# Kernel optimization log

Hardware: AMD Instinct MI355X
Metric: run time of the kernel (lower is better)

## Reference

```python
import jax, jax.numpy as jnp
import numpy as np

N, E, D, O = 50000, 800000, 128, 128
BN_EPS = 1e-5

def setup_inputs() -> dict:
    key = jax.random.key(0)
    ks = jax.random.split(key, 12)
    s1 = 1.0 / np.sqrt(D)
    s2 = 1.0 / np.sqrt(O)
    return {
        "x": jax.random.normal(ks[0], (N, D), dtype=jnp.float32),
        "edge_index": jax.random.randint(ks[1], (2, E), 0, N, dtype=jnp.int64),
        "batch": jnp.zeros((N,), dtype=jnp.int64),
        "eps": jnp.float32(0.0),  # GINConv train_eps parameter, init 0
        "W1": jax.random.uniform(ks[2], (O, D), jnp.float32, -s1, s1),
        "b1": jax.random.uniform(ks[3], (O,), jnp.float32, -s1, s1),
        "gamma1": jnp.ones((O,), jnp.float32),
        "beta1": jnp.zeros((O,), jnp.float32),
        "W2": jax.random.uniform(ks[4], (O, O), jnp.float32, -s2, s2),
        "b2": jax.random.uniform(ks[5], (O,), jnp.float32, -s2, s2),
        "gamma2": jnp.ones((O,), jnp.float32),
        "beta2": jnp.zeros((O,), jnp.float32),
    }

def _bn(h, gamma, beta):
    # BatchNorm1d training mode: biased variance over nodes
    m = jnp.mean(h, axis=0)
    v = jnp.var(h, axis=0)
    return (h - m) * jax.lax.rsqrt(v + BN_EPS) * gamma + beta

def reference(x, edge_index, batch, eps, W1, b1, gamma1, beta1, W2, b2, gamma2, beta2):
    src, dst = edge_index[0], edge_index[1]
    # sum_{j in N(i)} x_j  (scatter-add over edges)
    agg = jax.ops.segment_sum(x[src], dst, num_segments=N)
    h = (1.0 + eps) * x + agg
    h = jax.nn.relu(_bn(h @ W1.T + b1, gamma1, beta1))
    h = jax.nn.relu(_bn(h @ W2.T + b2, gamma2, beta2))
    return h
```

## Files before the change

kernel.cpp:

```cpp
#include <hip/hip_runtime.h>
#include <hip/hip_bf16.h>

typedef __hip_bfloat16 bf16;
typedef unsigned short u16;
typedef unsigned int u32;
typedef __attribute__((ext_vector_type(8))) short short8;
typedef __attribute__((ext_vector_type(4))) float floatx4;

#define N_NODES 50000
#define N_EDGES 800000
#define DIM 128
#define NB2 1563
#define NB2A 1792
#define CAP2 768
#define T_EDGES 4096

__device__ __forceinline__ u16 f2bfbits(float f) {
    bf16 h = __float2bfloat16(f);
    return *(u16*)&h;
}
__device__ __forceinline__ unsigned pack2(float a, float b) {
    return (unsigned)f2bfbits(a) | ((unsigned)f2bfbits(b) << 16);
}
__device__ __forceinline__ float lo2f(u32 u) { u32 v = u << 16; return __builtin_bit_cast(float, v); }
__device__ __forceinline__ float hi2f(u32 u) { u32 v = u & 0xFFFF0000u; return __builtin_bit_cast(float, v); }
__device__ __forceinline__ float b162f(u16 u) { u32 v = (u32)u << 16; return __builtin_bit_cast(float, v); }

__global__ void prep_kernel(const float* __restrict__ x, u32* __restrict__ xb,
                            const int* __restrict__ ei, int* __restrict__ flags,
                            int* __restrict__ gcur, float* __restrict__ stats) {
    int t = threadIdx.x;
    if (blockIdx.x == 0) {
        __shared__ int sdet;
        #pragma unroll
        for (int j = 0; j < 7; j++) {
            int i = j * 256 + t;
            if (i < NB2) gcur[i * 16] = 0;
        }
        #pragma unroll
        for (int j = 0; j < 16; j++) stats[j * 256 + t] = 0.f;
        if (t == 0) sdet = 0;
        __syncthreads();
        if (t < 64) { if (ei[2 * t + 1] != 0) atomicOr(&sdet, 1); }
        __syncthreads();
        if (t == 0) flags[1] = (sdet == 0) ? 1 : 0;
    }
    int i = (blockIdx.x * 256 + t) * 8;
    floatx4 v0 = *(const floatx4*)&x[i];
    floatx4 v1 = *(const floatx4*)&x[i + 4];
    uint4 r;
    r.x = pack2(v0[0], v0[1]); r.y = pack2(v0[2], v0[3]);
    r.z = pack2(v1[0], v1[1]); r.w = pack2(v1[2], v1[3]);
    *(uint4*)&xb[i / 2] = r;
}

__launch_bounds__(256)
__global__ void sort1_kernel(const int* __restrict__ ei, const int* __restrict__ flags,
                             u32* __restrict__ gbuck, int* __restrict__ gcur) {
    __shared__ int hist[NB2A];
    __shared__ int cur[NB2A];
    __shared__ int gbase[NB2A];
    int t = threadIdx.x;
    int is64 = flags[1];
    int e0 = blockIdx.x * T_EDGES;
    int n = N_EDGES - e0; if (n > T_EDGES) n = T_EDGES;

    for (int i = t; i < NB2A; i += 256) { hist[i] = 0; cur[i] = 0; }
    __syncthreads();

    u32 ed[T_EDGES / 256];
    #pragma unroll
    for (int j = 0; j < T_EDGES / 256; j++) {
        int idx = j * 256 + t;
        if (idx < n) {
            int e = e0 + idx;
            int js = e, jd = N_EDGES + e;
            if (is64) { js = 2 * e; jd = 2 * (N_EDGES + e); }
            u32 p = (u32)ei[js] | ((u32)ei[jd] << 16);
            ed[j] = p;
            atomicAdd(&hist[p >> 21], 1);
        }
    }
    __syncthreads();

    for (int i = t; i < NB2; i += 256) {
        int c = hist[i];
        gbase[i] = c ? atomicAdd(&gcur[i * 16], c) : 0;
    }
    __syncthreads();

    #pragma unroll
    for (int j = 0; j < T_EDGES / 256; j++) {
        int idx = j * 256 + t;
        if (idx < n) {
            u32 p = ed[j];
            int b = p >> 21;
            int pos = gbase[b] + atomicAdd(&cur[b], 1);
            gbuck[(long)b * CAP2 + pos] = p;
        }
    }
}

__launch_bounds__(256)
__global__ void sortagg_kernel(const u32* __restrict__ xb, const u32* __restrict__ gbuck,
                               const int* __restrict__ gcur, const float* __restrict__ epsp,
                               u32* __restrict__ hw) {
    __shared__ u32 sbuf[CAP2];
    __shared__ u16 slist[CAP2];
    __shared__ int cnt[32], offs[32], cur[32];
    int t = threadIdx.x, lane = t & 63, wv = t >> 6;
    int b = blockIdx.x;
    int n = gcur[b * 16]; if (n > CAP2) n = CAP2;
    long base = (long)b * CAP2;

    if (t < 32) { cnt[t] = 0; cur[t] = 0; }
    __syncthreads();
    for (int i = t; i < n; i += 256) {
        u32 p = gbuck[base + i];
        sbuf[i] = p;
        atomicAdd(&cnt[(p >> 16) & 31], 1);
    }
    __syncthreads();
    if (t < 32) {
        int v = cnt[t];
        int pv = v;
        #pragma unroll
        for (int d = 1; d < 32; d <<= 1) {
            int up = __shfl_up(pv, d);
            if (t >= d) pv += up;
        }
        offs[t] = pv - v;
    }
    __syncthreads();
    for (int i = t; i < n; i += 256) {
        u32 p = sbuf[i];
        int d = (p >> 16) & 31;
        int pos = offs[d] + atomicAdd(&cur[d], 1);
        slist[pos] = (u16)(p & 0xFFFF);
    }
    __syncthreads();

    float ep1 = 1.0f + epsp[0];
    for (int nn = wv; nn < 32; nn += 4) {
        int node = b * 32 + nn;
        if (node >= N_NODES) break;
        u32 self = xb[node * 64 + lane];
        float ax = ep1 * lo2f(self), ay = ep1 * hi2f(self);
        int s = offs[nn], e = s + cnt[nn];
        int i = s;
        for (; i + 16 <= e; i += 16) {
            int m[16];
            u32 u[16];
            #pragma unroll
            for (int j = 0; j < 16; j++) m[j] = slist[i + j];
            #pragma unroll
            for (int j = 0; j < 16; j++) u[j] = xb[m[j] * 64 + lane];
            #pragma unroll
            for (int j = 0; j < 16; j++) { ax += lo2f(u[j]); ay += hi2f(u[j]); }
        }
        for (; i + 8 <= e; i += 8) {
            int m[8];
            u32 u[8];
            #pragma unroll
            for (int j = 0; j < 8; j++) m[j] = slist[i + j];
            #pragma unroll
            for (int j = 0; j < 8; j++) u[j] = xb[m[j] * 64 + lane];
            #pragma unroll
            for (int j = 0; j < 8; j++) { ax += lo2f(u[j]); ay += hi2f(u[j]); }
        }
        for (; i + 2 <= e; i += 2) {
            u32 u0 = xb[(int)slist[i] * 64 + lane], u1 = xb[(int)slist[i + 1] * 64 + lane];
            ax += lo2f(u0) + lo2f(u1); ay += hi2f(u0) + hi2f(u1);
        }
        if (i < e) {
            u32 u = xb[(int)slist[i] * 64 + lane];
            ax += lo2f(u); ay += hi2f(u);
        }
        hw[node * 64 + lane] = pack2(ax, ay);
    }
}

template<int TRANSFORM>
__launch_bounds__(256)
__global__ void gemm_mfma(const u16* __restrict__ Ap, const float* __restrict__ Wp,
                          const float* __restrict__ bias,
                          const float* __restrict__ gamma, const float* __restrict__ beta,
                          const float* __restrict__ gstat,
                          u16* __restrict__ Yp, float* __restrict__ ostat) {
    __shared__ u16 sW[128 * 136];
    __shared__ float sScale[128], sShift[128], sBias[128], sSum[128], sSq[128];
    int t = threadIdx.x, lane = t & 63, wv = t >> 6;

    #pragma unroll
    for (int it = 0; it < 16; it++) {
        int q = it * 256 + t;
        int r = q >> 5, cq = q & 31;
        floatx4 w = ((const floatx4*)Wp)[q];
        u16 bb[4] = {f2bfbits(w[0]), f2bfbits(w[1]), f2bfbits(w[2]), f2bfbits(w[3])};
        *(uint2*)&sW[r * 136 + cq * 4] = *(uint2*)bb;
    }
    if (t < 128) {
        sSum[t] = 0.f; sSq[t] = 0.f; sBias[t] = bias[t];
        if (TRANSFORM) {
            float m = gstat[t * 16] * (1.0f / N_NODES);
            float v = fmaxf(gstat[t * 16 + 8] * (1.0f / N_NODES) - m * m, 0.0f);
            float rs = rsqrtf(v + 1e-5f);
            float sc = gamma[t] * rs;
            sScale[t] = sc;
            sShift[t] = beta[t] - m * sc;
        }
    }
    __syncthreads();

    int tile = blockIdx.x * 4 + wv;
    if (tile < (N_NODES / 16)) {
        int col0 = lane & 15, quad = lane >> 4;
        int mrow = tile * 16 + col0;

        short8 afr[4];
        #pragma unroll
        for (int ks = 0; ks < 4; ks++) {
            int kb = ks * 32 + quad * 8;
            short8 a = *(const short8*)&Ap[mrow * DIM + kb];
            if (TRANSFORM) {
                short8 r;
                #pragma unroll
                for (int j = 0; j < 8; j++) {
                    float f = b162f((u16)a[j]);
                    r[j] = (short)f2bfbits(fmaxf(fmaf(f, sScale[kb + j], sShift[kb + j]), 0.f));
                }
                afr[ks] = r;
            } else {
                afr[ks] = a;
            }
        }

        floatx4 acc[8];
        #pragma unroll
        for (int nt = 0; nt < 8; nt++) acc[nt] = (floatx4){0.f, 0.f, 0.f, 0.f};
        #pragma unroll
        for (int ks = 0; ks < 4; ks++) {
            #pragma unroll
            for (int nt = 0; nt < 8; nt++) {
                short8 bfr = *(const short8*)&sW[(nt * 16 + col0) * 136 + ks * 32 + quad * 8];
                acc[nt] = __builtin_amdgcn_mfma_f32_16x16x32_bf16(afr[ks], bfr, acc[nt], 0, 0, 0);
            }
        }

        #pragma unroll
        for (int nt = 0; nt < 8; nt++) {
            int col = nt * 16 + col0;
            float bb = sBias[col];
            float o0 = acc[nt][0] + bb, o1 = acc[nt][1] + bb;
            float o2 = acc[nt][2] + bb, o3 = acc[nt][3] + bb;
            int rbase = tile * 16 + quad * 4;
            Yp[(rbase + 0) * DIM + col] = f2bfbits(o0);
            Yp[(rbase + 1) * DIM + col] = f2bfbits(o1);
            Yp[(rbase + 2) * DIM + col] = f2bfbits(o2);
            Yp[(rbase + 3) * DIM + col] = f2bfbits(o3);
            float s = o0 + o1 + o2 + o3;
            float q = o0 * o0 + o1 * o1 + o2 * o2 + o3 * o3;
            s += __shfl_xor(s, 16); s += __shfl_xor(s, 32);
            q += __shfl_xor(q, 16); q += __shfl_xor(q, 32);
            if (quad == 0) { atomicAdd(&sSum[col], s); atomicAdd(&sSq[col], q); }
        }
    }
    __syncthreads();
    if (t < 128) {
        atomicAdd(&ostat[t * 16], sSum[t]);
        atomicAdd(&ostat[t * 16 + 8], sSq[t]);
    }
}

__global__ void output_kernel(const u32* __restrict__ Y,
                              const float* __restrict__ gstat,
                              const float* __restrict__ gamma, const float* __restrict__ beta,
                              float* __restrict__ out) {
    __shared__ float sScale[128], sShift[128];
    int t = threadIdx.x;
    if (t < 128) {
        float m = gstat[t * 16] * (1.0f / N_NODES);
        float v = fmaxf(gstat[t * 16 + 8] * (1.0f / N_NODES) - m * m, 0.0f);
        float rs = rsqrtf(v + 1e-5f);
        float sc = gamma[t] * rs;
        sScale[t] = sc;
        sShift[t] = beta[t] - m * sc;
    }
    __syncthreads();
    int i = (blockIdx.x * 256 + t) * 8;
    int c = i & 127;
    uint4 v = *(const uint4*)&Y[i / 2];
    u32 w[4] = {v.x, v.y, v.z, v.w};
    floatx4 o0, o1;
    #pragma unroll
    for (int j = 0; j < 4; j++) {
        float lo = lo2f(w[j]), hi = hi2f(w[j]);
        float r0 = fmaxf(fmaf(lo, sScale[c + 2 * j],     sShift[c + 2 * j]),     0.f);
        float r1 = fmaxf(fmaf(hi, sScale[c + 2 * j + 1], sShift[c + 2 * j + 1]), 0.f);
        if (j < 2) { o0[2 * j] = r0; o0[2 * j + 1] = r1; }
        else       { o1[2 * (j - 2)] = r0; o1[2 * (j - 2) + 1] = r1; }
    }
    *(floatx4*)&out[i] = o0;
    *(floatx4*)&out[i + 4] = o1;
}

extern "C" void kernel_launch(void* const* d_in, const int* in_sizes, int n_in,
                              void* d_out, int out_size, void* d_ws, size_t ws_size,
                              hipStream_t stream) {
    const float* x   = (const float*)d_in[0];
    const int* eraw  = (const int*)d_in[1];
    const float* eps = (const float*)d_in[3];
    const float* W1  = (const float*)d_in[4];
    const float* b1  = (const float*)d_in[5];
    const float* g1  = (const float*)d_in[6];
    const float* be1 = (const float*)d_in[7];
    const float* W2  = (const float*)d_in[8];
    const float* b2  = (const float*)d_in[9];
    const float* g2  = (const float*)d_in[10];
    const float* be2 = (const float*)d_in[11];

    char* ws = (char*)d_ws;
    size_t off = 0;
    u32* xb = (u32*)(ws + off);          off += (size_t)N_NODES * DIM * 2;
    u32* h1 = (u32*)(ws + off);          off += (size_t)N_NODES * DIM * 2;
    u16* y1 = (u16*)(ws + off);          off += (size_t)N_NODES * DIM * 2;
    u16* y2 = (u16*)(ws + off);          off += (size_t)N_NODES * DIM * 2;
    float* stats = (float*)(ws + off);   off += 4096 * 4;
    float* st1 = stats;
    float* st2 = stats + 2048;
    u32* gbuck = (u32*)(ws + off);       off += (size_t)NB2 * CAP2 * 4;
    int* gcur = (int*)(ws + off);        off += (size_t)((NB2 * 16 + 255) & ~255) * 4;
    int* flags = (int*)(ws + off);       off += 16 * 4;

    prep_kernel<<<N_NODES * DIM / (8 * 256), 256, 0, stream>>>(x, xb, eraw, flags, gcur, stats);
    sort1_kernel<<<(N_EDGES + T_EDGES - 1) / T_EDGES, 256, 0, stream>>>(eraw, flags, gbuck, gcur);
    sortagg_kernel<<<NB2, 256, 0, stream>>>(xb, gbuck, gcur, eps, h1);

    const int gemmGrid = (N_NODES / 16 + 3) / 4;
    gemm_mfma<0><<<gemmGrid, 256, 0, stream>>>((const u16*)h1, W1, b1,
                                               nullptr, nullptr, nullptr, y1, st1);
    gemm_mfma<1><<<gemmGrid, 256, 0, stream>>>(y1, W2, b2,
                                               g1, be1, st1, y2, st2);
    output_kernel<<<N_NODES * DIM / (8 * 256), 256, 0, stream>>>((const u32*)y2, st2,
                                                                 g2, be2, (float*)d_out);
}
```

Measured before the change: 259.0 us.

## Pre-convert weights to bf16 once and compute two row tiles per wave in GEMM

The prep kernel gets two extra blocks that write W1 and W2 as padded bf16 images. Each GEMM block then copies its weights into shared memory with plain vector loads instead of converting fp32 itself. The GEMM now has each wave handle two 16-row tiles, so every B fragment read from LDS feeds two MFMAs and the grid shrinks to 128 rows per block. The aggregation kernel also drops its 16-wide unrolled gather loop, which lowers register pressure but gives fewer loads in flight. The last GEMM block reads rows past the end of its input buffer, which lands in the next workspace buffer.

```diff
diff --git a/kernel.cpp b/kernel.cpp
--- a/kernel.cpp
+++ b/kernel.cpp
@@ -14,6 +14,8 @@
 #define NB2A 1792
 #define CAP2 768
 #define T_EDGES 4096
+#define WROW 136
+#define WIMG (128 * WROW)
 
 __device__ __forceinline__ u16 f2bfbits(float f) {
     bf16 h = __float2bfloat16(f);
@@ -28,9 +30,23 @@
 
 __global__ void prep_kernel(const float* __restrict__ x, u32* __restrict__ xb,
                             const int* __restrict__ ei, int* __restrict__ flags,
-                            int* __restrict__ gcur, float* __restrict__ stats) {
+                            int* __restrict__ gcur, float* __restrict__ stats,
+                            const float* __restrict__ W1, const float* __restrict__ W2,
+                            u16* __restrict__ w1i, u16* __restrict__ w2i) {
     int t = threadIdx.x;
-    if (blockIdx.x == 0) {
+    int bid = blockIdx.x;
+    if (bid >= 3125) {
+        const float* W = (bid == 3125) ? W1 : W2;
+        u16* wi = (bid == 3125) ? w1i : w2i;
+        #pragma unroll 4
+        for (int j = 0; j < 68; j++) {
+            int q = j * 256 + t;
+            int r = q / WROW, c = q - r * WROW;
+            wi[q] = (c < 128) ? f2bfbits(W[r * 128 + c]) : (u16)0;
+        }
+        return;
+    }
+    if (bid == 0) {
         __shared__ int sdet;
         #pragma unroll
         for (int j = 0; j < 7; j++) {
@@ -45,7 +61,7 @@
         __syncthreads();
         if (t == 0) flags[1] = (sdet == 0) ? 1 : 0;
     }
-    int i = (blockIdx.x * 256 + t) * 8;
+    int i = (bid * 256 + t) * 8;
     floatx4 v0 = *(const floatx4*)&x[i];
     floatx4 v1 = *(const floatx4*)&x[i + 4];
     uint4 r;
@@ -148,16 +164,6 @@
         float ax = ep1 * lo2f(self), ay = ep1 * hi2f(self);
         int s = offs[nn], e = s + cnt[nn];
         int i = s;
-        for (; i + 16 <= e; i += 16) {
-            int m[16];
-            u32 u[16];
-            #pragma unroll
-            for (int j = 0; j < 16; j++) m[j] = slist[i + j];
-            #pragma unroll
-            for (int j = 0; j < 16; j++) u[j] = xb[m[j] * 64 + lane];
-            #pragma unroll
-            for (int j = 0; j < 16; j++) { ax += lo2f(u[j]); ay += hi2f(u[j]); }
-        }
         for (; i + 8 <= e; i += 8) {
             int m[8];
             u32 u[8];
@@ -182,22 +188,22 @@
 
 template<int TRANSFORM>
 __launch_bounds__(256)
-__global__ void gemm_mfma(const u16* __restrict__ Ap, const float* __restrict__ Wp,
+__global__ void gemm_mfma(const u16* __restrict__ Ap, const u16* __restrict__ wimg,
                           const float* __restrict__ bias,
                           const float* __restrict__ gamma, const float* __restrict__ beta,
                           const float* __restrict__ gstat,
                           u16* __restrict__ Yp, float* __restrict__ ostat) {
-    __shared__ u16 sW[128 * 136];
+    __shared__ u16 sW[WIMG];
     __shared__ float sScale[128], sShift[128], sBias[128], sSum[128], sSq[128];
     int t = threadIdx.x, lane = t & 63, wv = t >> 6;
 
     #pragma unroll
-    for (int it = 0; it < 16; it++) {
+    for (int it = 0; it < 9; it++) {
         int q = it * 256 + t;
-        int r = q >> 5, cq = q & 31;
-        floatx4 w = ((const floatx4*)Wp)[q];
-        u16 bb[4] = {f2bfbits(w[0]), f2bfbits(w[1]), f2bfbits(w[2]), f2bfbits(w[3])};
-        *(uint2*)&sW[r * 136 + cq * 4] = *(uint2*)bb;
+        if (q < WIMG / 8) {
+            uint4 v = ((const uint4*)wimg)[q];
+            *(uint4*)&sW[q * 8] = v;
+        }
     }
     if (t < 128) {
         sSum[t] = 0.f; sSq[t] = 0.f; sBias[t] = bias[t];
@@ -212,48 +218,61 @@
     }
     __syncthreads();
 
-    int tile = blockIdx.x * 4 + wv;
-    if (tile < (N_NODES / 16)) {
-        int col0 = lane & 15, quad = lane >> 4;
-        int mrow = tile * 16 + col0;
-
-        short8 afr[4];
-        #pragma unroll
-        for (int ks = 0; ks < 4; ks++) {
-            int kb = ks * 32 + quad * 8;
-            short8 a = *(const short8*)&Ap[mrow * DIM + kb];
-            if (TRANSFORM) {
-                short8 r;
+    int col0 = lane & 15, quad = lane >> 4;
+    int row0 = blockIdx.x * 128 + wv * 32;
+
+    short8 afr[2][4];
+    #pragma unroll
+    for (int tt = 0; tt < 2; tt++) {
+        int mrow = row0 + tt * 16 + col0;
+        #pragma unroll
+        for (int ks = 0; ks < 4; ks++)
+            afr[tt][ks] = *(const short8*)&Ap[mrow * DIM + ks * 32 + quad * 8];
+    }
+    if (TRANSFORM) {
+        #pragma unroll
+        for (int tt = 0; tt < 2; tt++) {
+            #pragma unroll
+            for (int ks = 0; ks < 4; ks++) {
+                int kb = ks * 32 + quad * 8;
+                short8 a = afr[tt][ks], r;
                 #pragma unroll
                 for (int j = 0; j < 8; j++) {
                     float f = b162f((u16)a[j]);
                     r[j] = (short)f2bfbits(fmaxf(fmaf(f, sScale[kb + j], sShift[kb + j]), 0.f));
                 }
-                afr[ks] = r;
-            } else {
-                afr[ks] = a;
+                afr[tt][ks] = r;
             }
         }
-
-        floatx4 acc[8];
-        #pragma unroll
-        for (int nt = 0; nt < 8; nt++) acc[nt] = (floatx4){0.f, 0.f, 0.f, 0.f};
-        #pragma unroll
-        for (int ks = 0; ks < 4; ks++) {
-            #pragma unroll
-            for (int nt = 0; nt < 8; nt++) {
-                short8 bfr = *(const short8*)&sW[(nt * 16 + col0) * 136 + ks * 32 + quad * 8];
-                acc[nt] = __builtin_amdgcn_mfma_f32_16x16x32_bf16(afr[ks], bfr, acc[nt], 0, 0, 0);
-            }
-        }
-
+    }
+
+    floatx4 acc[2][8];
+    #pragma unroll
+    for (int tt = 0; tt < 2; tt++)
+        #pragma unroll
+        for (int nt = 0; nt < 8; nt++) acc[tt][nt] = (floatx4){0.f, 0.f, 0.f, 0.f};
+
+    #pragma unroll
+    for (int ks = 0; ks < 4; ks++) {
+        #pragma unroll
+        for (int nt = 0; nt < 8; nt++) {
+            short8 bfr = *(const short8*)&sW[(nt * 16 + col0) * WROW + ks * 32 + quad * 8];
+            acc[0][nt] = __builtin_amdgcn_mfma_f32_16x16x32_bf16(afr[0][ks], bfr, acc[0][nt], 0, 0, 0);
+            acc[1][nt] = __builtin_amdgcn_mfma_f32_16x16x32_bf16(afr[1][ks], bfr, acc[1][nt], 0, 0, 0);
+        }
+    }
+
+    #pragma unroll
+    for (int tt = 0; tt < 2; tt++) {
+        int rtile = row0 + tt * 16;
+        if (rtile >= N_NODES) break;
         #pragma unroll
         for (int nt = 0; nt < 8; nt++) {
             int col = nt * 16 + col0;
             float bb = sBias[col];
-            float o0 = acc[nt][0] + bb, o1 = acc[nt][1] + bb;
-            float o2 = acc[nt][2] + bb, o3 = acc[nt][3] + bb;
-            int rbase = tile * 16 + quad * 4;
+            float o0 = acc[tt][nt][0] + bb, o1 = acc[tt][nt][1] + bb;
+            float o2 = acc[tt][nt][2] + bb, o3 = acc[tt][nt][3] + bb;
+            int rbase = rtile + quad * 4;
             Yp[(rbase + 0) * DIM + col] = f2bfbits(o0);
             Yp[(rbase + 1) * DIM + col] = f2bfbits(o1);
             Yp[(rbase + 2) * DIM + col] = f2bfbits(o2);
@@ -328,18 +347,20 @@
     float* stats = (float*)(ws + off);   off += 4096 * 4;
     float* st1 = stats;
     float* st2 = stats + 2048;
+    u16* w1i = (u16*)(ws + off);         off += (size_t)WIMG * 2;
+    u16* w2i = (u16*)(ws + off);         off += (size_t)WIMG * 2;
     u32* gbuck = (u32*)(ws + off);       off += (size_t)NB2 * CAP2 * 4;
     int* gcur = (int*)(ws + off);        off += (size_t)((NB2 * 16 + 255) & ~255) * 4;
     int* flags = (int*)(ws + off);       off += 16 * 4;
 
-    prep_kernel<<<N_NODES * DIM / (8 * 256), 256, 0, stream>>>(x, xb, eraw, flags, gcur, stats);
+    prep_kernel<<<3127, 256, 0, stream>>>(x, xb, eraw, flags, gcur, stats, W1, W2, w1i, w2i);
     sort1_kernel<<<(N_EDGES + T_EDGES - 1) / T_EDGES, 256, 0, stream>>>(eraw, flags, gbuck, gcur);
     sortagg_kernel<<<NB2, 256, 0, stream>>>(xb, gbuck, gcur, eps, h1);
 
-    const int gemmGrid = (N_NODES / 16 + 3) / 4;
-    gemm_mfma<0><<<gemmGrid, 256, 0, stream>>>((const u16*)h1, W1, b1,
+    const int gemmGrid = (N_NODES + 127) / 128;
+    gemm_mfma<0><<<gemmGrid, 256, 0, stream>>>((const u16*)h1, w1i, b1,
                                                nullptr, nullptr, nullptr, y1, st1);
-    gemm_mfma<1><<<gemmGrid, 256, 0, stream>>>(y1, W2, b2,
+    gemm_mfma<1><<<gemmGrid, 256, 0, stream>>>(y1, w2i, b2,
                                                g1, be1, st1, y2, st2);
     output_kernel<<<N_NODES * DIM / (8 * 256), 256, 0, stream>>>((const u32*)y2, st2,
                                                                  g2, be2, (float*)d_out);
```

Measured after the change: 240.4 us. -7.2%, faster.
